# Kernel optimization log

Hardware: AMD Instinct MI355X
Metric: run time of the kernel (lower is better)

## Reference

```python
import jax, jax.numpy as jnp
import numpy as np

D_MODEL = 1024
N_HEADS = 16
HEAD = D_MODEL // N_HEADS  # 64
B, S = 4, 2048


def setup_inputs() -> dict:
    key = jax.random.key(0)
    ks = jax.random.split(key, 8)
    sd = 1.0 / np.sqrt(D_MODEL)
    return {
        "query": jax.random.normal(ks[0], (B, S, D_MODEL), jnp.float32),
        "key_in": jax.random.normal(ks[1], (B, S, D_MODEL), jnp.float32),
        "value": jax.random.normal(ks[2], (B, S, D_MODEL), jnp.float32),
        # per-head projections stacked: [H, d_model, head_size]
        "Wq": jax.random.normal(ks[3], (N_HEADS, D_MODEL, HEAD), jnp.float32) * sd,
        "Wk": jax.random.normal(ks[4], (N_HEADS, D_MODEL, HEAD), jnp.float32) * sd,
        "Wv": jax.random.normal(ks[5], (N_HEADS, D_MODEL, HEAD), jnp.float32) * sd,
        "Wo": jax.random.normal(ks[6], (D_MODEL, D_MODEL), jnp.float32) * sd,
        "bo": jax.random.normal(ks[7], (D_MODEL,), jnp.float32) * 0.01,
    }


def reference(query, key_in, value, Wq, Wk, Wv, Wo, bo):
    # batched per-head projections: [B,H,S,K]
    q = jnp.einsum("bsd,hdk->bhsk", query, Wq)
    k = jnp.einsum("bsd,hdk->bhsk", key_in, Wk)
    v = jnp.einsum("bsd,hdk->bhsk", value, Wv)
    # NOTE: original scales by sqrt(d_model) (query.shape[-1]), not sqrt(head_size)
    scale = 1.0 / np.sqrt(D_MODEL)
    scores = jnp.einsum("bhsk,bhtk->bhst", q, k) * scale  # [B,H,S,S]
    attn = jax.nn.softmax(scores, axis=-1)
    ctx = jnp.einsum("bhst,bhtk->bhsk", attn, v)  # [B,H,S,K]
    # concat heads -> [B,S,H*K]
    ctx = jnp.transpose(ctx, (0, 2, 1, 3)).reshape(B, S, D_MODEL)
    return ctx @ Wo.T + bo  # output linear (dropout = identity at eval)
```

## Files before the change

### kernel.cpp

```cpp
#include <hip/hip_runtime.h>
#include <stdint.h>

#define DM   1024
#define HD   64
#define SEQ  2048
#define NB   4
#define MR   8192

typedef __bf16  bf16x8 __attribute__((ext_vector_type(8)));
typedef float   f32x4  __attribute__((ext_vector_type(4)));
typedef unsigned short u16x8 __attribute__((ext_vector_type(8)));

__device__ __forceinline__ unsigned short f2bf(float f) {
  union { float f; unsigned u; } x; x.f = f;
  unsigned u = x.u + 0x7fffu + ((x.u >> 16) & 1u);
  return (unsigned short)(u >> 16);
}

__device__ __forceinline__ unsigned pk_trunc(float a, float b) {
  unsigned ua = __builtin_bit_cast(unsigned, a);
  unsigned ub = __builtin_bit_cast(unsigned, b);
  return __builtin_amdgcn_perm(ub, ua, 0x07060302);
}

__device__ __forceinline__ float fexp2(float x) {
#if __has_builtin(__builtin_amdgcn_exp2f)
  return __builtin_amdgcn_exp2f(x);
#else
  float r; asm("v_exp_f32 %0, %1" : "=v"(r) : "v"(x)); return r;
#endif
}

__device__ __forceinline__ void gld_lds16(const void* g, void* l) {
  __builtin_amdgcn_global_load_lds((const __attribute__((address_space(1))) unsigned int*)g,
                                   (__attribute__((address_space(3))) unsigned int*)l, 16, 0, 0);
}

__global__ __launch_bounds__(256) void prep(
    const float* __restrict__ qf32, const float* __restrict__ kf32, const float* __restrict__ vf32,
    unsigned short* __restrict__ xq, unsigned short* __restrict__ xk, unsigned short* __restrict__ xv,
    const float* __restrict__ wq, const float* __restrict__ wk, const float* __restrict__ wv,
    unsigned short* __restrict__ wt, const float* __restrict__ wo, unsigned short* __restrict__ wob) {
  __shared__ float tile[64 * 65];
  const int z = blockIdx.z, tid = threadIdx.x;
  if (z < 3) {
    const float* in = (z == 0) ? qf32 : (z == 1) ? kf32 : vf32;
    unsigned short* out = (z == 0) ? xq : (z == 1) ? xk : xv;
    size_t i = ((size_t)blockIdx.x * 256 + tid) * 8;
    float4 x = *(const float4*)(in + i);
    float4 y = *(const float4*)(in + i + 4);
    u16x8 r = { f2bf(x.x), f2bf(x.y), f2bf(x.z), f2bf(x.w), f2bf(y.x), f2bf(y.y), f2bf(y.z), f2bf(y.w) };
    *(u16x8*)(out + i) = r;
    return;
  }
  const int bx = blockIdx.x;
  if (bx < 768) {
    const int zz = bx >> 8, bb = bx & 255;
    const float* in = (zz == 0) ? wq : (zz == 1) ? wk : wv;
    unsigned short* out = wt + ((size_t)zz << 20);
    const int h = bb >> 4, d0 = (bb & 15) * 64;
    const int k = tid & 63, rr = tid >> 6;
#pragma unroll
    for (int j = 0; j < 16; ++j) {
      int row = rr + j * 4;
      tile[row * 65 + k] = in[h * 65536 + (d0 + row) * 64 + k];
    }
    __syncthreads();
    const int dd = tid & 63, kr = tid >> 6;
#pragma unroll
    for (int j = 0; j < 16; ++j) {
      int k2 = kr + j * 4;
      out[(size_t)(h * 64 + k2) * 1024 + d0 + dd] = f2bf(tile[dd * 65 + k2]);
    }
  } else if (bx < 1280) {
    size_t i = ((size_t)(bx - 768) * 256 + tid) * 8;
    float4 x = *(const float4*)(wo + i);
    float4 y = *(const float4*)(wo + i + 4);
    u16x8 r = { f2bf(x.x), f2bf(x.y), f2bf(x.z), f2bf(x.w), f2bf(y.x), f2bf(y.y), f2bf(y.z), f2bf(y.w) };
    *(u16x8*)(wob + i) = r;
  }
}

template <bool BF16OUT>
__global__ __launch_bounds__(256, 2) void gemm_bt(
    const unsigned short* __restrict__ A0, const unsigned short* __restrict__ A1,
    const unsigned short* __restrict__ A2, const unsigned short* __restrict__ Bt,
    void* __restrict__ Cv, const float* __restrict__ bias) {
  __shared__ char lds[65536];

  const int tid = threadIdx.x, w = tid >> 6, l = tid & 63;
  const int quad = l >> 4, l15 = l & 15;
  const int z = blockIdx.z;
  const unsigned short* A = (z == 0) ? A0 : (z == 1) ? A1 : A2;
  const unsigned short* B = Bt + (size_t)z * (DM * DM);
  const int lin = blockIdx.y * 8 + blockIdx.x;
  const int swz = (lin & 7) * 64 + (lin >> 3);
  const int bm = (swz >> 3) * 128, bn = (swz & 7) * 128;
  const int wrow = (w >> 1) * 64, wcol = (w & 1) * 64;

  const int srow = w * 32 + (l >> 3);
  const int sc   = ((l & 7) ^ ((l >> 3) & 7)) * 8;

  f32x4 acc[4][4];
#pragma unroll
  for (int i = 0; i < 4; ++i)
#pragma unroll
    for (int j = 0; j < 4; ++j) acc[i][j] = (f32x4){0.f, 0.f, 0.f, 0.f};

#define STAGEG(buf, kt) do {                                                   \
    char* dA = lds + (buf) * 32768 + (w * 32) * 128;                           \
    char* dB = dA + 16384;                                                     \
    _Pragma("unroll")                                                          \
    for (int p = 0; p < 4; ++p) {                                              \
      gld_lds16(A + (size_t)(bm + srow + p * 8) * DM + (kt) + sc, dA + p * 1024); \
      gld_lds16(B + (size_t)(bn + srow + p * 8) * DM + (kt) + sc, dB + p * 1024); \
    } } while (0)

  STAGEG(0, 0);
  __syncthreads();
  int cur = 0;

  for (int kt = 0; kt < DM; kt += 64) {
    if (kt + 64 < DM) STAGEG(cur ^ 1, kt + 64);
    char* ldsA = lds + cur * 32768;
    char* ldsB = ldsA + 16384;
#pragma unroll
    for (int ks = 0; ks < 2; ++ks) {
      const int x = ((ks * 4 + quad) ^ (l15 & 7)) * 16;
      const char* abase = ldsA + (wrow + l15) * 128 + x;
      const char* bbase = ldsB + (wcol + l15) * 128 + x;
      bf16x8 af[4], bfr[4];
#pragma unroll
      for (int mt = 0; mt < 4; ++mt) af[mt] = *(const bf16x8*)(abase + mt * 2048);
#pragma unroll
      for (int nt = 0; nt < 4; ++nt) bfr[nt] = *(const bf16x8*)(bbase + nt * 2048);
#pragma unroll
      for (int mt = 0; mt < 4; ++mt)
#pragma unroll
        for (int nt = 0; nt < 4; ++nt)
          acc[mt][nt] = __builtin_amdgcn_mfma_f32_16x16x32_bf16(af[mt], bfr[nt], acc[mt][nt], 0, 0, 0);
    }
    __syncthreads();
    cur ^= 1;
  }
#undef STAGEG

  if constexpr (BF16OUT) {
    unsigned short* C = (unsigned short*)Cv + (size_t)z * ((size_t)MR * DM);
#pragma unroll
    for (int mt = 0; mt < 4; ++mt)
#pragma unroll
      for (int r = 0; r < 4; ++r) {
        size_t row = bm + wrow + mt * 16 + quad * 4 + r;
#pragma unroll
        for (int nt = 0; nt < 4; ++nt)
          C[row * DM + bn + wcol + nt * 16 + l15] = f2bf(acc[mt][nt][r]);
      }
  } else {
    float* C = (float*)Cv;
    float bv[4];
#pragma unroll
    for (int nt = 0; nt < 4; ++nt) bv[nt] = bias[bn + wcol + nt * 16 + l15];
#pragma unroll
    for (int mt = 0; mt < 4; ++mt)
#pragma unroll
      for (int r = 0; r < 4; ++r) {
        size_t row = bm + wrow + mt * 16 + quad * 4 + r;
#pragma unroll
        for (int nt = 0; nt < 4; ++nt)
          C[row * DM + bn + wcol + nt * 16 + l15] = acc[mt][nt][r] + bv[nt];
      }
  }
}

__global__ __launch_bounds__(512, 4) void attn_flash(
    const unsigned short* __restrict__ Qp, const unsigned short* __restrict__ Kp,
    const unsigned short* __restrict__ Vp, unsigned short* __restrict__ Ctx) {
  __shared__ char lds[65536];
  char* ldsK  = lds;
  char* ldsVt = lds + 16384;
  char* ldsP  = lds + 32768;

  const int tid = threadIdx.x, w = tid >> 6, l = tid & 63;
  const int quad = l >> 4, l15 = l & 15;
  const int lin = blockIdx.y * 8 + blockIdx.x;
  const int swz = (lin & 7) * 64 + (lin >> 3);
  const int qt = swz & 7, bh = swz >> 3;
  const int b = bh >> 4, h = bh & 15;
  const size_t rb = (size_t)b * SEQ;
  const int hc = h * HD;

  bf16x8 qf[2][2];
  const int q0 = qt * 256 + w * 32;
#pragma unroll
  for (int mt = 0; mt < 2; ++mt)
#pragma unroll
    for (int ks = 0; ks < 2; ++ks)
      qf[mt][ks] = *(const bf16x8*)(Qp + (rb + q0 + mt * 16 + l15) * DM + hc + ks * 32 + quad * 8);

  f32x4 o[2][4], l_acc[2];
#pragma unroll
  for (int mt = 0; mt < 2; ++mt) {
    l_acc[mt] = (f32x4){0.f, 0.f, 0.f, 0.f};
#pragma unroll
    for (int nt = 0; nt < 4; ++nt) o[mt][nt] = (f32x4){0.f, 0.f, 0.f, 0.f};
  }

  const int sc = ((l & 7) ^ (l >> 3)) * 8;
  const float c2 = 0.045084220027780106f;
  char* prow = ldsP + w * 4096;

  const u16x8 ones_u = {0x3f80, 0x3f80, 0x3f80, 0x3f80, 0x3f80, 0x3f80, 0x3f80, 0x3f80};
  const bf16x8 ones = __builtin_bit_cast(bf16x8, ones_u);

  {
    gld_lds16(Kp + (rb + w * 8 + (l >> 3)) * DM + hc + sc, ldsK + w * 1024);
    u16x8 vr = *(const u16x8*)(Vp + (rb + l) * DM + hc + w * 8);
#pragma unroll
    for (int i = 0; i < 8; ++i) {
      int n = w * 8 + i;
      *(unsigned short*)(ldsVt + n * 128 + (((l >> 3) ^ i) * 16) + (l & 7) * 2) = vr[i];
    }
  }

  for (int kt = 0; kt < SEQ / 64; ++kt) {
    const int kb = kt & 1;
    char* ldsKb = ldsK + kb * 8192;
    char* ldsVb = ldsVt + kb * 8192;
    __syncthreads();

    u16x8 vr;
    const bool pre = (kt < SEQ / 64 - 1);
    if (pre) {
      const size_t krow = rb + (size_t)(kt + 1) * 64;
      gld_lds16(Kp + (krow + w * 8 + (l >> 3)) * DM + hc + sc, ldsK + (kb ^ 1) * 8192 + w * 1024);
      vr = *(const u16x8*)(Vp + (krow + l) * DM + hc + w * 8);
    }

    f32x4 s[2][4];
#pragma unroll
    for (int mt = 0; mt < 2; ++mt)
#pragma unroll
      for (int ct = 0; ct < 4; ++ct) s[mt][ct] = (f32x4){0.f, 0.f, 0.f, 0.f};
    __builtin_amdgcn_s_setprio(1);
#pragma unroll
    for (int ks = 0; ks < 2; ++ks) {
      const int x = ((ks * 4 + quad) ^ (l15 & 7)) * 16;
      const char* kbase = ldsKb + l15 * 128 + x;
#pragma unroll
      for (int ct = 0; ct < 4; ++ct) {
        bf16x8 kf = *(const bf16x8*)(kbase + ct * 2048);
        s[0][ct] = __builtin_amdgcn_mfma_f32_16x16x32_bf16(kf, qf[0][ks], s[0][ct], 0, 0, 0);
        s[1][ct] = __builtin_amdgcn_mfma_f32_16x16x32_bf16(kf, qf[1][ks], s[1][ct], 0, 0, 0);
      }
    }
    __builtin_amdgcn_s_setprio(0);

#pragma unroll
    for (int mt = 0; mt < 2; ++mt) {
      char* pr = prow + (mt * 16 + l15) * 128;
      const int co = quad >> 1, bo = (quad & 1) * 8;
#pragma unroll
      for (int ct = 0; ct < 4; ++ct) {
        float p0 = fexp2(__builtin_fmaf(s[mt][ct][0], c2, -2.0f));
        float p1 = fexp2(__builtin_fmaf(s[mt][ct][1], c2, -2.0f));
        float p2 = fexp2(__builtin_fmaf(s[mt][ct][2], c2, -2.0f));
        float p3 = fexp2(__builtin_fmaf(s[mt][ct][3], c2, -2.0f));
        unsigned lo = pk_trunc(p0, p1), hi = pk_trunc(p2, p3);
        unsigned long long pw = (unsigned long long)lo | ((unsigned long long)hi << 32);
        int c = 2 * ct + co;
        *(unsigned long long*)(pr + ((c ^ (l15 & 7)) * 16) + bo) = pw;
      }
    }

    __builtin_amdgcn_s_setprio(1);
#pragma unroll
    for (int ks = 0; ks < 2; ++ks) {
      const int x = ((ks * 4 + quad) ^ (l15 & 7)) * 16;
      const char* pbase = prow + l15 * 128 + x;
      const char* vbase = ldsVb + l15 * 128 + x;
      bf16x8 pf0 = *(const bf16x8*)(pbase);
      bf16x8 pf1 = *(const bf16x8*)(pbase + 2048);
      l_acc[0] = __builtin_amdgcn_mfma_f32_16x16x32_bf16(pf0, ones, l_acc[0], 0, 0, 0);
      l_acc[1] = __builtin_amdgcn_mfma_f32_16x16x32_bf16(pf1, ones, l_acc[1], 0, 0, 0);
#pragma unroll
      for (int nt = 0; nt < 4; ++nt) {
        bf16x8 vf = *(const bf16x8*)(vbase + nt * 2048);
        o[0][nt] = __builtin_amdgcn_mfma_f32_16x16x32_bf16(pf0, vf, o[0][nt], 0, 0, 0);
        o[1][nt] = __builtin_amdgcn_mfma_f32_16x16x32_bf16(pf1, vf, o[1][nt], 0, 0, 0);
      }
    }
    __builtin_amdgcn_s_setprio(0);

    if (pre) {
      char* vb = ldsVt + (kb ^ 1) * 8192;
#pragma unroll
      for (int i = 0; i < 8; ++i) {
        int n = w * 8 + i;
        *(unsigned short*)(vb + n * 128 + (((l >> 3) ^ i) * 16) + (l & 7) * 2) = vr[i];
      }
    }
  }

#pragma unroll
  for (int mt = 0; mt < 2; ++mt) {
#pragma unroll
    for (int r = 0; r < 4; ++r) {
      float inv = 1.f / l_acc[mt][r];
      size_t row = rb + q0 + mt * 16 + quad * 4 + r;
#pragma unroll
      for (int nt = 0; nt < 4; ++nt)
        Ctx[row * DM + hc + nt * 16 + l15] = f2bf(o[mt][nt][r] * inv);
    }
  }
}

extern "C" void kernel_launch(void* const* d_in, const int* in_sizes, int n_in,
                              void* d_out, int out_size, void* d_ws, size_t ws_size,
                              hipStream_t stream) {
  const float* query  = (const float*)d_in[0];
  const float* key_in = (const float*)d_in[1];
  const float* value  = (const float*)d_in[2];
  const float* Wq = (const float*)d_in[3];
  const float* Wk = (const float*)d_in[4];
  const float* Wv = (const float*)d_in[5];
  const float* Wo = (const float*)d_in[6];
  const float* bo = (const float*)d_in[7];
  float* out = (float*)d_out;

  unsigned short* ws = (unsigned short*)d_ws;
  const size_t NT = (size_t)MR * DM;
  unsigned short* Xq  = ws;
  unsigned short* Xk  = Xq + NT;
  unsigned short* Xv  = Xk + NT;
  unsigned short* Wt  = Xv + NT;
  unsigned short* Wob = Wt + 3 * 1048576;
  unsigned short* Qb  = Wob + 1048576;
  unsigned short* Kb  = Qb + NT;
  unsigned short* Vb  = Kb + NT;
  unsigned short* Cx  = Vb + NT;

  prep<<<dim3(4096, 1, 4), 256, 0, stream>>>(query, key_in, value, Xq, Xk, Xv,
                                             Wq, Wk, Wv, Wt, Wo, Wob);
  gemm_bt<true><<<dim3(8, 64, 3), 256, 0, stream>>>(Xq, Xk, Xv, Wt, Qb, nullptr);
  attn_flash<<<dim3(8, 64), 512, 0, stream>>>(Qb, Kb, Vb, Cx);
  gemm_bt<false><<<dim3(8, 64, 1), 256, 0, stream>>>(Cx, Cx, Cx, Wob, out, bo);
}
```

Before: 294.4 us.

## Fuse fp32-to-bf16 activation conversion into the QKV projection GEMM loads

The prep kernel no longer converts query/key/value to bf16 in workspace buffers. The QKV GEMM instead loads the fp32 activations directly, converts them in registers and writes them into LDS with the same swizzled layout. This removes a full write and re-read of three bf16 activation copies, and shrinks the prep launch to the weight work only. In exchange, the A-tile path gives up the asynchronous global-to-LDS load for synchronous register loads, which could expose memory latency in the GEMM main loop. Each GEMM block also now reads twice as many bytes of A per tile.

Measured after the change: 337.5 us. 14.6% more time.

```diff
diff --git a/kernel.cpp b/kernel.cpp
--- a/kernel.cpp
+++ b/kernel.cpp
@@ -37,23 +37,10 @@
 }
 
 __global__ __launch_bounds__(256) void prep(
-    const float* __restrict__ qf32, const float* __restrict__ kf32, const float* __restrict__ vf32,
-    unsigned short* __restrict__ xq, unsigned short* __restrict__ xk, unsigned short* __restrict__ xv,
     const float* __restrict__ wq, const float* __restrict__ wk, const float* __restrict__ wv,
     unsigned short* __restrict__ wt, const float* __restrict__ wo, unsigned short* __restrict__ wob) {
   __shared__ float tile[64 * 65];
-  const int z = blockIdx.z, tid = threadIdx.x;
-  if (z < 3) {
-    const float* in = (z == 0) ? qf32 : (z == 1) ? kf32 : vf32;
-    unsigned short* out = (z == 0) ? xq : (z == 1) ? xk : xv;
-    size_t i = ((size_t)blockIdx.x * 256 + tid) * 8;
-    float4 x = *(const float4*)(in + i);
-    float4 y = *(const float4*)(in + i + 4);
-    u16x8 r = { f2bf(x.x), f2bf(x.y), f2bf(x.z), f2bf(x.w), f2bf(y.x), f2bf(y.y), f2bf(y.z), f2bf(y.w) };
-    *(u16x8*)(out + i) = r;
-    return;
-  }
-  const int bx = blockIdx.x;
+  const int bx = blockIdx.x, tid = threadIdx.x;
   if (bx < 768) {
     const int zz = bx >> 8, bb = bx & 255;
     const float* in = (zz == 0) ? wq : (zz == 1) ? wk : wv;
@@ -81,10 +68,12 @@
   }
 }
 
-template <bool BF16OUT>
+template <bool BF16OUT, bool CVTA>
 __global__ __launch_bounds__(256, 2) void gemm_bt(
     const unsigned short* __restrict__ A0, const unsigned short* __restrict__ A1,
-    const unsigned short* __restrict__ A2, const unsigned short* __restrict__ Bt,
+    const unsigned short* __restrict__ A2,
+    const float* __restrict__ F0, const float* __restrict__ F1, const float* __restrict__ F2,
+    const unsigned short* __restrict__ Bt,
     void* __restrict__ Cv, const float* __restrict__ bias) {
   __shared__ char lds[65536];
 
@@ -92,6 +81,7 @@
   const int quad = l >> 4, l15 = l & 15;
   const int z = blockIdx.z;
   const unsigned short* A = (z == 0) ? A0 : (z == 1) ? A1 : A2;
+  const float* F = (z == 0) ? F0 : (z == 1) ? F1 : F2;
   const unsigned short* B = Bt + (size_t)z * (DM * DM);
   const int lin = blockIdx.y * 8 + blockIdx.x;
   const int swz = (lin & 7) * 64 + (lin >> 3);
@@ -112,7 +102,16 @@
     char* dB = dA + 16384;                                                     \
     _Pragma("unroll")                                                          \
     for (int p = 0; p < 4; ++p) {                                              \
-      gld_lds16(A + (size_t)(bm + srow + p * 8) * DM + (kt) + sc, dA + p * 1024); \
+      if constexpr (CVTA) {                                                    \
+        size_t e = (size_t)(bm + srow + p * 8) * DM + (kt) + sc;               \
+        float4 x = *(const float4*)(F + e);                                    \
+        float4 y = *(const float4*)(F + e + 4);                                \
+        u16x8 r = { f2bf(x.x), f2bf(x.y), f2bf(x.z), f2bf(x.w),                \
+                    f2bf(y.x), f2bf(y.y), f2bf(y.z), f2bf(y.w) };              \
+        *(u16x8*)(dA + p * 1024 + l * 16) = r;                                 \
+      } else {                                                                 \
+        gld_lds16(A + (size_t)(bm + srow + p * 8) * DM + (kt) + sc, dA + p * 1024); \
+      }                                                                        \
       gld_lds16(B + (size_t)(bn + srow + p * 8) * DM + (kt) + sc, dB + p * 1024); \
     } } while (0)
 
@@ -310,7 +309,7 @@
       size_t row = rb + q0 + mt * 16 + quad * 4 + r;
 #pragma unroll
       for (int nt = 0; nt < 4; ++nt)
-        Ctx[row * DM + hc + nt * 16 + l15] = f2bf(o[mt][nt][r] * inv);
+        Ctx[row * DM + hc + nt * 16 + l15] = f2bf(o[nt == 0 ? mt : mt][nt][r] * inv);
     }
   }
 }
@@ -330,19 +329,17 @@
 
   unsigned short* ws = (unsigned short*)d_ws;
   const size_t NT = (size_t)MR * DM;
-  unsigned short* Xq  = ws;
-  unsigned short* Xk  = Xq + NT;
-  unsigned short* Xv  = Xk + NT;
-  unsigned short* Wt  = Xv + NT;
+  unsigned short* Wt  = ws;
   unsigned short* Wob = Wt + 3 * 1048576;
   unsigned short* Qb  = Wob + 1048576;
   unsigned short* Kb  = Qb + NT;
   unsigned short* Vb  = Kb + NT;
   unsigned short* Cx  = Vb + NT;
 
-  prep<<<dim3(4096, 1, 4), 256, 0, stream>>>(query, key_in, value, Xq, Xk, Xv,
-                                             Wq, Wk, Wv, Wt, Wo, Wob);
-  gemm_bt<true><<<dim3(8, 64, 3), 256, 0, stream>>>(Xq, Xk, Xv, Wt, Qb, nullptr);
+  prep<<<dim3(1280, 1, 1), 256, 0, stream>>>(Wq, Wk, Wv, Wt, Wo, Wob);
+  gemm_bt<true, true><<<dim3(8, 64, 3), 256, 0, stream>>>(
+      nullptr, nullptr, nullptr, query, key_in, value, Wt, Qb, nullptr);
   attn_flash<<<dim3(8, 64), 512, 0, stream>>>(Qb, Kb, Vb, Cx);
-  gemm_bt<false><<<dim3(8, 64, 1), 256, 0, stream>>>(Cx, Cx, Cx, Wob, out, bo);
-}
+  gemm_bt<false, false><<<dim3(8, 64, 1), 256, 0, stream>>>(
+      Cx, Cx, Cx, nullptr, nullptr, nullptr, Wob, out, bo);
+}
```
